# Kernel tuning notes

Hardware: AMD Instinct MI355X
Metric: run time of the kernel (lower is better)

The kernel has to match this reference:

```python
import jax, jax.numpy as jnp
import numpy as np

B, T, C = 2, 2048, 2048
E, K, S, F = 8, 2, 1, 1408
AUX_COEF, Z_COEF = 0.01, 0.001


def setup_inputs() -> dict:
    key = jax.random.key(0)
    ks = jax.random.split(key, 8)
    sc = 1.0 / np.sqrt(C)
    sf = 1.0 / np.sqrt(F)
    return {
        "x": jax.random.normal(ks[0], (B, T, C), jnp.float32),
        "gate_w": jax.random.normal(ks[1], (E, C), jnp.float32) * sc,   # torch Linear weight [out,in]
        "w1": jax.random.normal(ks[2], (E, F, C), jnp.float32) * sc,    # routed expert up-proj
        "w2": jax.random.normal(ks[3], (E, C, F), jnp.float32) * sf,    # routed expert down-proj
        "sw1": jax.random.normal(ks[4], (S, F, C), jnp.float32) * sc,   # shared expert up-proj
        "sw2": jax.random.normal(ks[5], (S, C, F), jnp.float32) * sf,   # shared expert down-proj
        "alpha": jnp.ones((C,), jnp.float32),                            # HyperConnection scale on MoE out
        "beta": jnp.ones((C,), jnp.float32),                             # HyperConnection scale on residual x
    }


def reference(x, gate_w, w1, w2, sw1, sw2, alpha, beta):
    Bv, Tv, Cv = x.shape
    xf = x.reshape(-1, Cv)                                  # [N, C]
    logits = xf @ gate_w.T                                  # [N, E]
    probs = jax.nn.softmax(logits, axis=-1)
    weights, selected = jax.lax.top_k(probs, K)             # [N, K]
    weights = weights / jnp.sum(weights, axis=-1, keepdims=True)
    aux_loss = AUX_COEF * jnp.sum(jnp.mean(probs, axis=0) ** 2)
    z_loss = Z_COEF * jnp.mean(jax.nn.logsumexp(logits, axis=-1) ** 2)
    # combine[n, e] = routing weight of expert e for token n (0 if not selected)
    combine = jnp.sum(jax.nn.one_hot(selected, E, dtype=xf.dtype) * weights[..., None], axis=1)  # [N, E]
    out = jnp.zeros_like(xf)
    for e in range(E):  # fixed small expert count; weight is 0 for unrouted tokens
        h = jax.nn.silu(xf @ w1[e].T) @ w2[e].T             # [N, C]
        out = out + combine[:, e:e + 1] * h
    for s in range(S):
        out = out + jax.nn.silu(xf @ sw1[s].T) @ sw2[s].T
    y = alpha * out.reshape(Bv, Tv, Cv) + beta * x           # HyperConnection residual mix
    return y, aux_loss + z_loss
```

## Files before the change

kernel.cpp:

```cpp
#include <hip/hip_runtime.h>


#define TOKS 4096
#define CD 2048
#define FD 1408
#define FDP 1536
#define RROWS 8192
#define NT256 56

typedef unsigned short u16;
typedef float f32x4 __attribute__((ext_vector_type(4)));
typedef __bf16 bf16x8 __attribute__((ext_vector_type(8)));

__device__ __forceinline__ u16 f2bf(float f) {
  unsigned u = __float_as_uint(f);
  u += 0x7fffu + ((u >> 16) & 1u);
  return (u16)(u >> 16);
}

__global__ __launch_bounds__(256) void gate_kernel(
    const float* __restrict__ x, const float* __restrict__ gw,
    float* __restrict__ combine, float* __restrict__ part, int* __restrict__ sel,
    u16* __restrict__ xb)
{
  const int lane = threadIdx.x & 63;
  const int wave = threadIdx.x >> 6;
  const int n = blockIdx.x * 4 + wave;
  const float* xr = x + (size_t)n * CD;
  u16* xbr = xb + (size_t)n * CD;
  float p[8] = {0,0,0,0,0,0,0,0};
#pragma unroll
  for (int it = 0; it < 8; ++it) {
    const int idx = it * 256 + lane * 4;
    const float4 xv = *(const float4*)(xr + idx);
    ushort4 xo;
    xo.x = f2bf(xv.x); xo.y = f2bf(xv.y); xo.z = f2bf(xv.z); xo.w = f2bf(xv.w);
    *(ushort4*)(xbr + idx) = xo;
#pragma unroll
    for (int e = 0; e < 8; ++e) {
      const float4 gv = *(const float4*)(gw + e * CD + idx);
      p[e] += xv.x * gv.x + xv.y * gv.y + xv.z * gv.z + xv.w * gv.w;
    }
  }
#pragma unroll
  for (int e = 0; e < 8; ++e) {
#pragma unroll
    for (int m = 32; m > 0; m >>= 1) p[e] += __shfl_xor(p[e], m, 64);
  }
  float mx = p[0];
#pragma unroll
  for (int e = 1; e < 8; ++e) mx = fmaxf(mx, p[e]);
  float s = 0.f, pr[8];
#pragma unroll
  for (int e = 0; e < 8; ++e) { pr[e] = __expf(p[e] - mx); s += pr[e]; }
  const float inv = 1.f / s;
#pragma unroll
  for (int e = 0; e < 8; ++e) pr[e] *= inv;
  const float lse = mx + __logf(s);
  int i1 = 0;
#pragma unroll
  for (int e = 1; e < 8; ++e) if (pr[e] > pr[i1]) i1 = e;
  int i2 = (i1 == 0) ? 1 : 0;
#pragma unroll
  for (int e = 0; e < 8; ++e) if (e != i1 && pr[e] > pr[i2]) i2 = e;
  const float rs = 1.f / (pr[i1] + pr[i2]);

  __shared__ float pl[4][12];
  if (lane == 0) {
    float* cr = combine + (size_t)n * 16;
#pragma unroll
    for (int e = 0; e < 8; ++e) cr[e] = 0.f;
    cr[i1] = pr[i1] * rs;
    cr[i2] = pr[i2] * rs;
    cr[8] = 1.0f;
    sel[n] = i1 | (i2 << 4);
#pragma unroll
    for (int e = 0; e < 8; ++e) pl[wave][e] = pr[e];
    pl[wave][8] = lse * lse;
  }
  __syncthreads();
  if (threadIdx.x < 9)
    part[(size_t)blockIdx.x * 16 + threadIdx.x] =
        pl[0][threadIdx.x] + pl[1][threadIdx.x] + pl[2][threadIdx.x] + pl[3][threadIdx.x];
}

__global__ void route_kernel(const int* __restrict__ sel, int* __restrict__ le,
                             int* __restrict__ pos, int* __restrict__ cntoff,
                             int* __restrict__ tileMap)
{
  const int lane = threadIdx.x;
  const unsigned long long lt = (1ull << lane) - 1ull;
  int cnt[8] = {0,0,0,0,0,0,0,0};
  for (int c = 0; c < TOKS / 64; ++c) {
    const int s = sel[c * 64 + lane];
    const int e1 = s & 15, e2 = (s >> 4) & 15;
#pragma unroll
    for (int e = 0; e < 8; ++e)
      cnt[e] += __popcll(__ballot(e1 == e)) + __popcll(__ballot(e2 == e));
  }
  int off[8]; off[0] = 0;
#pragma unroll
  for (int e = 1; e < 8; ++e) off[e] = off[e - 1] + cnt[e - 1];
  int base[8];
#pragma unroll
  for (int e = 0; e < 8; ++e) base[e] = off[e];
  for (int c = 0; c < TOKS / 64; ++c) {
    const int n = c * 64 + lane;
    const int s = sel[n];
    const int e1 = s & 15, e2 = (s >> 4) & 15;
#pragma unroll
    for (int e = 0; e < 8; ++e) {
      const unsigned long long m1 = __ballot(e1 == e);
      const unsigned long long m2 = __ballot(e2 == e);
      if (e1 == e) { const int r = base[e] + __popcll(m1 & lt); le[r] = n; pos[2 * n] = r; }
      if (e2 == e) { const int r = base[e] + __popcll(m1) + __popcll(m2 & lt); le[r] = n; pos[2 * n + 1] = r; }
      base[e] += __popcll(m1) + __popcll(m2);
    }
  }
  if (lane < 8) { cntoff[lane] = cnt[lane]; cntoff[16 + lane] = off[lane]; }
  if (lane == 8) { cntoff[8] = TOKS; cntoff[24] = RROWS; }
  if (lane == 0) {
    int t = 0;
    for (int e = 0; e < 8; ++e)
      for (int m = 0; m < cnt[e]; m += 256) tileMap[t++] = e | (m << 4);
    for (int m = 0; m < TOKS; m += 256) tileMap[t++] = 8 | (m << 4);
    cntoff[25] = t;
  }
}

__global__ void finalize_kernel(const float* __restrict__ part, float* __restrict__ loss_out)
{
  __shared__ float sm[256][10];
  float loc[9] = {0,0,0,0,0,0,0,0,0};
  for (int b = threadIdx.x; b < 1024; b += 256)
#pragma unroll
    for (int c = 0; c < 9; ++c) loc[c] += part[(size_t)b * 16 + c];
#pragma unroll
  for (int c = 0; c < 9; ++c) sm[threadIdx.x][c] = loc[c];
  __syncthreads();
  for (int off = 128; off > 0; off >>= 1) {
    if (threadIdx.x < off)
#pragma unroll
      for (int c = 0; c < 9; ++c) sm[threadIdx.x][c] += sm[threadIdx.x + off][c];
    __syncthreads();
  }
  if (threadIdx.x == 0) {
    float aux = 0.f;
#pragma unroll
    for (int e = 0; e < 8; ++e) { const float m = sm[0][e] * (1.f / TOKS); aux += m * m; }
    const float z = sm[0][8] * (1.f / TOKS);
    loss_out[0] = 0.01f * aux + 0.001f * z;
  }
}

#define S1E  786432
#define S2E  720896
__global__ void cast_all_kernel(const float* __restrict__ w1, const float* __restrict__ sw1,
                                const float* __restrict__ w2, const float* __restrict__ sw2,
                                u16* __restrict__ w1b, u16* __restrict__ w2b)
{
  const int total = 9 * (S1E + S2E);
  int i = blockIdx.x * blockDim.x + threadIdx.x;
  const int stride = gridDim.x * blockDim.x;
  for (; i < total; i += stride) {
    ushort4 o;
    u16* dst;
    if (i < 9 * S1E) {
      const int e = i / S1E, rem = i - e * S1E;
      const int r = rem >> 9, g = rem & 511;
      dst = w1b + ((size_t)e * FDP + r) * CD + g * 4;
      if (r < FD) {
        const float* src = (e < 8) ? (w1 + ((size_t)e * FD + r) * CD) : (sw1 + (size_t)r * CD);
        const float4 v = *(const float4*)(src + g * 4);
        o.x = f2bf(v.x); o.y = f2bf(v.y); o.z = f2bf(v.z); o.w = f2bf(v.w);
      } else {
        o.x = o.y = o.z = o.w = 0;
      }
    } else {
      const int j = i - 9 * S1E;
      const int e = j / S2E, rem = j - e * S2E;
      const int r = rem / 352, g = rem % 352;
      const float* src = (e < 8) ? (w2 + ((size_t)e * CD + r) * FD) : (sw2 + (size_t)r * FD);
      const float4 v = *(const float4*)(src + g * 4);
      o.x = f2bf(v.x); o.y = f2bf(v.y); o.z = f2bf(v.z); o.w = f2bf(v.w);
      dst = w2b + ((size_t)e * CD + r) * FD + g * 4;
    }
    *(ushort4*)dst = o;
  }
}


template<int MODE>
__global__ __launch_bounds__(512, 2) void gemm8p(
    const u16* __restrict__ Abase, const u16* __restrict__ Bbase,
    u16* __restrict__ outBF, const float* __restrict__ combine,
    const int* __restrict__ le, const int* __restrict__ cntoff,
    const int* __restrict__ tileMap)
{
  constexpr int K   = (MODE == 0) ? CD : FD;
  constexpr int BS  = (MODE == 0) ? FDP : CD;
  constexpr int OS  = (MODE == 0) ? FD : CD;
  constexpr int NY  = (MODE == 0) ? 6 : 8;
  constexpr int NKT = K >> 6;
  constexpr int Q   = NT256 * NY / 8;

  __shared__ __attribute__((aligned(16))) u16 smA[2][256 * 64];
  __shared__ __attribute__((aligned(16))) u16 smB[2][256 * 64];

  const int orig = blockIdx.x + gridDim.x * blockIdx.y;
  const int wgid = (orig & 7) * Q + (orig >> 3);
  const int tix = wgid / NY;
  const int y = wgid - tix * NY;
  const int NT = cntoff[25];
  if (tix >= NT) return;
  const int packed = tileMap[tix];
  const int e = packed & 15;
  const int m0 = packed >> 4;
  const int cnt = cntoff[e];
  const int off = cntoff[16 + e];
  const int n0 = y * 256;

  const int tid  = threadIdx.x;
  const int ln   = tid & 63;
  const int wv   = tid >> 6;
  const int wm   = wv >> 2;
  const int wn   = wv & 3;
  const int la15 = ln & 15;
  const int g16  = ln >> 4;

  const u16* Bp = Bbase + (size_t)e * (size_t)BS * K;

  const int rx  = la15 & 7;
  const int go0 = ((g16 ^ rx) << 3);
  const int go1 = (((4 + g16) ^ rx) << 3);
  const int abase = wm * 128 + la15;
  const int bbase = wn * 64 + la15;

  const int srow = ln >> 3;
  const int sgrp = (((ln & 7) ^ srow) << 3);
  const u16* pA[2][2];
  const u16* pB[2][2];
#pragma unroll
  for (int h = 0; h < 2; ++h)
#pragma unroll
    for (int l = 0; l < 2; ++l) {
      const int rloc = h * 128 + (wv * 2 + l) * 8 + srow;
      size_t arow;
      if (MODE == 0)
        arow = (e == 8) ? (size_t)(m0 + rloc)
                        : (size_t)le[min(off + m0 + rloc, RROWS - 1)];
      else
        arow = (size_t)(off + m0 + rloc);
      pA[h][l] = Abase + arow * K + sgrp;
      pB[h][l] = Bp + (size_t)(n0 + h * 128 + (wv * 2 + l) * 8 + srow) * K + sgrp;
    }

#define SA(buf, kt)                                                                           \
  _Pragma("unroll")                                                                           \
  for (int h_ = 0; h_ < 2; ++h_)                                                              \
    _Pragma("unroll")                                                                         \
    for (int l_ = 0; l_ < 2; ++l_)                                                            \
      __builtin_amdgcn_global_load_lds(                                                       \
          (const __attribute__((address_space(1))) void*)(pA[h_][l_] + (kt) * 64),            \
          (__attribute__((address_space(3))) void*)(&smA[buf][h_ * 8192 + (wv * 2 + l_) * 512]),\
          16, 0, 0);
#define SB(buf, kt)                                                                           \
  _Pragma("unroll")                                                                           \
  for (int h_ = 0; h_ < 2; ++h_)                                                              \
    _Pragma("unroll")                                                                         \
    for (int l_ = 0; l_ < 2; ++l_)                                                            \
      __builtin_amdgcn_global_load_lds(                                                       \
          (const __attribute__((address_space(1))) void*)(pB[h_][l_] + (kt) * 64),            \
          (__attribute__((address_space(3))) void*)(&smB[buf][h_ * 8192 + (wv * 2 + l_) * 512]),\
          16, 0, 0);

#define BAR()  { asm volatile("" ::: "memory"); __builtin_amdgcn_s_barrier(); asm volatile("" ::: "memory"); }
#define LGK0() { asm volatile("s_waitcnt lgkmcnt(0)" ::: "memory"); __builtin_amdgcn_sched_barrier(0); }

#define RDA(mq)                                                                               \
  { const u16* s_ = &smA[cur][0];                                                             \
    _Pragma("unroll")                                                                         \
    for (int i_ = 0; i_ < 4; ++i_) {                                                          \
      const int r_ = abase + (mq) * 64 + i_ * 16;                                             \
      a[i_][0] = *(const bf16x8*)(s_ + r_ * 64 + go0);                                        \
      a[i_][1] = *(const bf16x8*)(s_ + r_ * 64 + go1);                                        \
    } }
#define RDB(nq, dst)                                                                          \
  { const u16* s_ = &smB[cur][0];                                                             \
    _Pragma("unroll")                                                                         \
    for (int j_ = 0; j_ < 2; ++j_) {                                                          \
      const int r_ = bbase + (nq) * 32 + j_ * 16;                                             \
      dst[j_][0] = *(const bf16x8*)(s_ + r_ * 64 + go0);                                      \
      dst[j_][1] = *(const bf16x8*)(s_ + r_ * 64 + go1);                                      \
    } }
#define MM(mq, nq, bb)                                                                        \
  { __builtin_amdgcn_s_setprio(1);                                                            \
    _Pragma("unroll")                                                                         \
    for (int kk_ = 0; kk_ < 2; ++kk_)                                                         \
      _Pragma("unroll")                                                                       \
      for (int i_ = 0; i_ < 4; ++i_)                                                          \
        _Pragma("unroll")                                                                     \
        for (int j_ = 0; j_ < 2; ++j_)                                                        \
          acc[(mq) * 4 + i_][(nq) * 2 + j_] = __builtin_amdgcn_mfma_f32_16x16x32_bf16(        \
              a[i_][kk_], bb[j_][kk_], acc[(mq) * 4 + i_][(nq) * 2 + j_], 0, 0, 0);           \
    __builtin_amdgcn_s_setprio(0); }

  f32x4 acc[8][4] = {};
  bf16x8 a[4][2], b0[2][2], b1[2][2];

  SA(0, 0) SB(0, 0)
  asm volatile("s_waitcnt vmcnt(0)" ::: "memory");
  BAR()

#pragma unroll 1
  for (int T = 0; T < NKT; ++T) {
    const int cur = T & 1;
    const int nxt = cur ^ 1;
    if (T + 1 < NKT) SA(nxt, T + 1)
    RDA(0) RDB(0, b0)
    BAR() LGK0() MM(0, 0, b0) BAR()
    if (T + 1 < NKT) SB(nxt, T + 1)
    RDB(1, b1)
    BAR() LGK0() MM(0, 1, b1) BAR()
    RDA(1)
    BAR() LGK0() MM(1, 1, b1) BAR()
    MM(1, 0, b0)
    asm volatile("s_waitcnt vmcnt(0)" ::: "memory");
    BAR()
  }

#undef SA
#undef SB
#undef BAR
#undef LGK0
#undef RDA
#undef RDB
#undef MM

#pragma unroll
  for (int mi = 0; mi < 8; ++mi) {
    const int rq = wm * 128 + (mi >> 2) * 64 + (mi & 3) * 16 + g16 * 4;
#pragma unroll
    for (int q = 0; q < 4; ++q) {
      const int rloc = rq + q;
      if (m0 + rloc >= cnt) continue;
      float sc = 1.f;
      if (MODE == 0) {
        const int tok = (e == 8) ? (m0 + rloc) : le[off + m0 + rloc];
        sc = combine[(size_t)tok * 16 + e];
      }
#pragma unroll
      for (int ni = 0; ni < 4; ++ni) {
        const int col = n0 + wn * 64 + (ni >> 1) * 32 + (ni & 1) * 16 + la15;
        if (MODE == 0 && col >= FD) continue;
        const float v = acc[mi][ni][q];
        const float h = (MODE == 0) ? (sc * v * (1.f / (1.f + __expf(-v)))) : v;
        outBF[(size_t)(off + m0 + rloc) * OS + col] = f2bf(h);
      }
    }
  }
}

__global__ __launch_bounds__(256) void gather_kernel(
    const u16* __restrict__ Yc, const int* __restrict__ pos,
    const float* __restrict__ x, const float* __restrict__ alpha,
    const float* __restrict__ beta, float* __restrict__ out)
{
  const int n = blockIdx.x;
  const int c0 = threadIdx.x * 8;
  const int p1 = pos[2 * n], p2 = pos[2 * n + 1];
  const bf16x8 a = *(const bf16x8*)(Yc + (size_t)p1 * CD + c0);
  const bf16x8 b = *(const bf16x8*)(Yc + (size_t)p2 * CD + c0);
  const bf16x8 s = *(const bf16x8*)(Yc + ((size_t)RROWS + n) * CD + c0);
  const float* xr = x + (size_t)n * CD + c0;
  float* orow = out + (size_t)n * CD + c0;
#pragma unroll
  for (int j = 0; j < 8; ++j) {
    const float v = (float)a[j] + (float)b[j] + (float)s[j];
    orow[j] = alpha[c0 + j] * v + beta[c0 + j] * xr[j];
  }
}

extern "C" void kernel_launch(void* const* d_in, const int* in_sizes, int n_in,
                              void* d_out, int out_size, void* d_ws, size_t ws_size,
                              hipStream_t stream)
{
  (void)in_sizes; (void)n_in; (void)out_size; (void)ws_size;
  const float* x     = (const float*)d_in[0];
  const float* gw    = (const float*)d_in[1];
  const float* w1    = (const float*)d_in[2];
  const float* w2    = (const float*)d_in[3];
  const float* sw1   = (const float*)d_in[4];
  const float* sw2   = (const float*)d_in[5];
  const float* alpha = (const float*)d_in[6];
  const float* beta  = (const float*)d_in[7];
  float* out = (float*)d_out;

  char* ws = (char*)d_ws;
  float* combine = (float*)(ws + 0);
  float* part    = (float*)(ws + 262144);
  int*   sel     = (int*)(ws + 327680);
  int*   le      = (int*)(ws + 344064);
  int*   pos     = (int*)(ws + 376832);
  int*   cntoff  = (int*)(ws + 409600);
  int*   tileMap = (int*)(ws + 409856);
  u16*   xb      = (u16*)(ws + 410368);
  u16*   w1b     = (u16*)(ws + 17187584);
  u16*   w2b     = (u16*)(ws + 73810688);
  u16*   Hcomp   = (u16*)(ws + 125715200);
  u16*   Ycomp   = (u16*)(ws + 160318208);

  gate_kernel<<<1024, 256, 0, stream>>>(x, gw, combine, part, sel, xb);
  route_kernel<<<1, 64, 0, stream>>>(sel, le, pos, cntoff, tileMap);
  finalize_kernel<<<1, 256, 0, stream>>>(part, out + (size_t)TOKS * CD);
  cast_all_kernel<<<4096, 256, 0, stream>>>(w1, sw1, w2, sw2, w1b, w2b);
  gemm8p<0><<<dim3(NT256, 6), 512, 0, stream>>>(xb, w1b, Hcomp, combine, le, cntoff, tileMap);
  gemm8p<1><<<dim3(NT256, 8), 512, 0, stream>>>(Hcomp, w2b, Ycomp, nullptr, nullptr, cntoff, tileMap);
  gather_kernel<<<TOKS, 256, 0, stream>>>(Ycomp, pos, x, alpha, beta, out);
}
```

Baseline: 502.8 us.

## Split tile loads into half-tiles and pipeline with partial vmcnt waits

The GEMM main loop now issues the next k-tile's global-to-LDS loads in four half-tile pieces interleaved with the MFMA phases, waiting only with vmcnt(4) instead of draining all loads at the end of each iteration. The warp-to-tile mapping is remapped so each MFMA quadrant depends only on one half of A and B in LDS, which lets compute start before the whole tile has arrived. Several barriers are removed and the epilogue row and column indexing is updated to match the new mapping. This aims to hide global load latency and cut barrier stalls, at the cost of more delicate hazard ordering; on the last iteration it also issues redundant loads of tile 0.

Result: faster. 422.7 us (-15.9%).

```diff
diff --git a/kernel.cpp b/kernel.cpp
--- a/kernel.cpp
+++ b/kernel.cpp
@@ -233,8 +233,6 @@
   const int rx  = la15 & 7;
   const int go0 = ((g16 ^ rx) << 3);
   const int go1 = (((4 + g16) ^ rx) << 3);
-  const int abase = wm * 128 + la15;
-  const int bbase = wn * 64 + la15;
 
   const int srow = ln >> 3;
   const int sgrp = (((ln & 7) ^ srow) << 3);
@@ -255,33 +253,30 @@
       pB[h][l] = Bp + (size_t)(n0 + h * 128 + (wv * 2 + l) * 8 + srow) * K + sgrp;
     }
 
-#define SA(buf, kt)                                                                           \
+#define SA1(buf, h, kt)                                                                       \
   _Pragma("unroll")                                                                           \
-  for (int h_ = 0; h_ < 2; ++h_)                                                              \
-    _Pragma("unroll")                                                                         \
-    for (int l_ = 0; l_ < 2; ++l_)                                                            \
-      __builtin_amdgcn_global_load_lds(                                                       \
-          (const __attribute__((address_space(1))) void*)(pA[h_][l_] + (kt) * 64),            \
-          (__attribute__((address_space(3))) void*)(&smA[buf][h_ * 8192 + (wv * 2 + l_) * 512]),\
-          16, 0, 0);
-#define SB(buf, kt)                                                                           \
+  for (int l_ = 0; l_ < 2; ++l_)                                                              \
+    __builtin_amdgcn_global_load_lds(                                                         \
+        (const __attribute__((address_space(1))) void*)(pA[h][l_] + (kt) * 64),               \
+        (__attribute__((address_space(3))) void*)(&smA[buf][(h) * 8192 + (wv * 2 + l_) * 512]),\
+        16, 0, 0);
+#define SB1(buf, h, kt)                                                                       \
   _Pragma("unroll")                                                                           \
-  for (int h_ = 0; h_ < 2; ++h_)                                                              \
-    _Pragma("unroll")                                                                         \
-    for (int l_ = 0; l_ < 2; ++l_)                                                            \
-      __builtin_amdgcn_global_load_lds(                                                       \
-          (const __attribute__((address_space(1))) void*)(pB[h_][l_] + (kt) * 64),            \
-          (__attribute__((address_space(3))) void*)(&smB[buf][h_ * 8192 + (wv * 2 + l_) * 512]),\
-          16, 0, 0);
+  for (int l_ = 0; l_ < 2; ++l_)                                                              \
+    __builtin_amdgcn_global_load_lds(                                                         \
+        (const __attribute__((address_space(1))) void*)(pB[h][l_] + (kt) * 64),               \
+        (__attribute__((address_space(3))) void*)(&smB[buf][(h) * 8192 + (wv * 2 + l_) * 512]),\
+        16, 0, 0);
 
 #define BAR()  { asm volatile("" ::: "memory"); __builtin_amdgcn_s_barrier(); asm volatile("" ::: "memory"); }
 #define LGK0() { asm volatile("s_waitcnt lgkmcnt(0)" ::: "memory"); __builtin_amdgcn_sched_barrier(0); }
+#define VM4()  { asm volatile("s_waitcnt vmcnt(4)" ::: "memory"); }
 
 #define RDA(mq)                                                                               \
   { const u16* s_ = &smA[cur][0];                                                             \
     _Pragma("unroll")                                                                         \
     for (int i_ = 0; i_ < 4; ++i_) {                                                          \
-      const int r_ = abase + (mq) * 64 + i_ * 16;                                             \
+      const int r_ = (mq) * 128 + wm * 64 + i_ * 16 + la15;                                   \
       a[i_][0] = *(const bf16x8*)(s_ + r_ * 64 + go0);                                        \
       a[i_][1] = *(const bf16x8*)(s_ + r_ * 64 + go1);                                        \
     } }
@@ -289,7 +284,7 @@
   { const u16* s_ = &smB[cur][0];                                                             \
     _Pragma("unroll")                                                                         \
     for (int j_ = 0; j_ < 2; ++j_) {                                                          \
-      const int r_ = bbase + (nq) * 32 + j_ * 16;                                             \
+      const int r_ = (nq) * 128 + wn * 32 + j_ * 16 + la15;                                   \
       dst[j_][0] = *(const bf16x8*)(s_ + r_ * 64 + go0);                                      \
       dst[j_][1] = *(const bf16x8*)(s_ + r_ * 64 + go1);                                      \
     } }
@@ -308,38 +303,41 @@
   f32x4 acc[8][4] = {};
   bf16x8 a[4][2], b0[2][2], b1[2][2];
 
-  SA(0, 0) SB(0, 0)
-  asm volatile("s_waitcnt vmcnt(0)" ::: "memory");
+  SA1(0, 0, 0) SB1(0, 0, 0) SB1(0, 1, 0) SA1(0, 1, 0)
+  VM4()
   BAR()
 
 #pragma unroll 1
   for (int T = 0; T < NKT; ++T) {
     const int cur = T & 1;
     const int nxt = cur ^ 1;
-    if (T + 1 < NKT) SA(nxt, T + 1)
+    const int kn = (T + 1 < NKT) ? (T + 1) : 0;
     RDA(0) RDB(0, b0)
-    BAR() LGK0() MM(0, 0, b0) BAR()
-    if (T + 1 < NKT) SB(nxt, T + 1)
+    SA1(nxt, 0, kn)
+    VM4() BAR() LGK0() MM(0, 0, b0)
     RDB(1, b1)
-    BAR() LGK0() MM(0, 1, b1) BAR()
+    SB1(nxt, 0, kn)
+    VM4() BAR() LGK0() MM(0, 1, b1)
     RDA(1)
-    BAR() LGK0() MM(1, 1, b1) BAR()
-    MM(1, 0, b0)
-    asm volatile("s_waitcnt vmcnt(0)" ::: "memory");
-    BAR()
-  }
-
-#undef SA
-#undef SB
+    SB1(nxt, 1, kn)
+    BAR() LGK0() MM(1, 1, b1)
+    SA1(nxt, 1, kn)
+    VM4() BAR() MM(1, 0, b0)
+  }
+  asm volatile("s_waitcnt vmcnt(0)" ::: "memory");
+
+#undef SA1
+#undef SB1
 #undef BAR
 #undef LGK0
+#undef VM4
 #undef RDA
 #undef RDB
 #undef MM
 
 #pragma unroll
   for (int mi = 0; mi < 8; ++mi) {
-    const int rq = wm * 128 + (mi >> 2) * 64 + (mi & 3) * 16 + g16 * 4;
+    const int rq = (mi >> 2) * 128 + wm * 64 + (mi & 3) * 16 + g16 * 4;
 #pragma unroll
     for (int q = 0; q < 4; ++q) {
       const int rloc = rq + q;
@@ -351,7 +349,7 @@
       }
 #pragma unroll
       for (int ni = 0; ni < 4; ++ni) {
-        const int col = n0 + wn * 64 + (ni >> 1) * 32 + (ni & 1) * 16 + la15;
+        const int col = n0 + (ni >> 1) * 128 + wn * 32 + (ni & 1) * 16 + la15;
         if (MODE == 0 && col >= FD) continue;
         const float v = acc[mi][ni][q];
         const float h = (MODE == 0) ? (sc * v * (1.f / (1.f + __expf(-v)))) : v;
```
